# Performance work log

Hardware: AMD Instinct MI355X
Metric: run time of the kernel (lower is better)

The kernel has to match this reference:

```python
import jax, jax.numpy as jnp
import numpy as np

EMB = 1024
FF = 4 * EMB

def _ternary(w):
    # BitNet b1.58 absmean quantization; forward uses pure ternary weights
    scale = jnp.maximum(jnp.mean(jnp.abs(w)), 1e-8)
    w_t = jnp.clip(jnp.round(w / scale), -1.0, 1.0)
    # STE: forward = w_t, backward = identity w.r.t. w
    return w + jax.lax.stop_gradient(w_t - w)

def setup_inputs() -> dict:
    key = jax.random.key(0)
    kx, k1, k2, kb1, kb2 = jax.random.split(key, 5)
    x = jax.random.normal(kx, (4, 2048, EMB), dtype=jnp.float32)
    # nn.Linear default init: U(-1/sqrt(fan_in), 1/sqrt(fan_in))
    lim1 = 1.0 / np.sqrt(EMB)
    lim2 = 1.0 / np.sqrt(FF)
    W1 = jax.random.uniform(k1, (FF, EMB), jnp.float32, -lim1, lim1)
    b1 = jax.random.uniform(kb1, (FF,), jnp.float32, -lim1, lim1)
    W2 = jax.random.uniform(k2, (EMB, FF), jnp.float32, -lim2, lim2)
    b2 = jax.random.uniform(kb2, (EMB,), jnp.float32, -lim2, lim2)
    return {"x": x, "W1": W1, "b1": b1, "W2": W2, "b2": b2}

def reference(x, W1, b1, W2, b2):
    h = jnp.einsum('bsd,fd->bsf', x, _ternary(W1)) + b1  # [B,S,FF]
    h = jax.nn.gelu(h, approximate=False)  # torch nn.GELU default = exact erf
    out = jnp.einsum('bsf,df->bsd', h, _ternary(W2)) + b2  # [B,S,EMB]
    return out
```

## Files before the change

kernel.cpp:

```cpp
#include <hip/hip_runtime.h>
#include <hip/hip_bf16.h>
#include <cstdint>
#include <cstddef>

typedef __bf16 bf16x8 __attribute__((ext_vector_type(8)));
typedef float  f32x4  __attribute__((ext_vector_type(4)));

__device__ __forceinline__ unsigned short f2bf(float f) {
    __hip_bfloat16 b = __float2bfloat16(f);
    return *reinterpret_cast<unsigned short*>(&b);
}

__device__ __forceinline__ float fast_gelu(float x) {
    float x2 = x * x;
    float m  = x * __builtin_fmaf(x2, -0.10294314f, -2.30220795f);
    float e  = __builtin_amdgcn_exp2f(m);
    return x * __builtin_amdgcn_rcpf(1.0f + e);
}


__global__ void abs_sum_cvt_kernel(const float4* __restrict__ w0, const float4* __restrict__ w1,
                                   int n4w, float* __restrict__ part,
                                   const float4* __restrict__ x, ushort4* __restrict__ xb,
                                   int n4x) {
    int seg = (int)blockIdx.x >> 9;
    int b = (int)blockIdx.x & 511;
    if (seg == 2) {
        for (int i = b * blockDim.x + threadIdx.x; i < n4x; i += 512 * blockDim.x) {
            float4 v = x[i];
            ushort4 o;
            o.x = f2bf(v.x); o.y = f2bf(v.y); o.z = f2bf(v.z); o.w = f2bf(v.w);
            xb[i] = o;
        }
        return;
    }
    const float4* w = seg ? w1 : w0;
    float s = 0.0f;
    for (int i = b * blockDim.x + threadIdx.x; i < n4w; i += 512 * blockDim.x) {
        float4 v = w[i];
        s += fabsf(v.x) + fabsf(v.y) + fabsf(v.z) + fabsf(v.w);
    }
    #pragma unroll
    for (int o = 32; o > 0; o >>= 1) s += __shfl_down(s, o, 64);
    __shared__ float ps[4];
    int lane = threadIdx.x & 63, wid = threadIdx.x >> 6;
    if (lane == 0) ps[wid] = s;
    __syncthreads();
    if (threadIdx.x == 0) part[blockIdx.x] = ps[0] + ps[1] + ps[2] + ps[3];
}

__global__ void ternarize_kernel(const float4* __restrict__ w0, ushort4* __restrict__ t0,
                                 const float4* __restrict__ w1, ushort4* __restrict__ t1,
                                 int n4w, const float* __restrict__ part, float inv_n) {
    int seg = (int)blockIdx.x >> 10;
    int b = (int)blockIdx.x & 1023;

    float s = 0.0f;
    for (int j = threadIdx.x; j < 512; j += 256) s += part[seg * 512 + j];
    #pragma unroll
    for (int o = 32; o > 0; o >>= 1) s += __shfl_down(s, o, 64);
    __shared__ float ps[4];
    __shared__ float sscale;
    int lane = threadIdx.x & 63, wid = threadIdx.x >> 6;
    if (lane == 0) ps[wid] = s;
    __syncthreads();
    if (threadIdx.x == 0) {
        float tot = ps[0] + ps[1] + ps[2] + ps[3];
        sscale = fmaxf(tot * inv_n, 1e-8f);
    }
    __syncthreads();
    float inv = 1.0f / sscale;

    const float4* w = seg ? w1 : w0;
    ushort4* t = seg ? t1 : t0;
    for (int i = b * blockDim.x + threadIdx.x; i < n4w; i += 1024 * blockDim.x) {
        float4 v = w[i];
        ushort4 o;
        o.x = f2bf(fminf(fmaxf(rintf(v.x * inv), -1.0f), 1.0f));
        o.y = f2bf(fminf(fmaxf(rintf(v.y * inv), -1.0f), 1.0f));
        o.z = f2bf(fminf(fmaxf(rintf(v.z * inv), -1.0f), 1.0f));
        o.w = f2bf(fminf(fmaxf(rintf(v.w * inv), -1.0f), 1.0f));
        t[i] = o;
    }
}


#define GLL(SRC, DST) __builtin_amdgcn_global_load_lds( \
    (const __attribute__((address_space(1))) void*)(SRC), \
    (__attribute__((address_space(3))) void*)(DST), 16, 0, 0)

#define BAR() do { asm volatile("" ::: "memory"); \
    __builtin_amdgcn_sched_barrier(0); \
    __builtin_amdgcn_s_barrier(); \
    __builtin_amdgcn_sched_barrier(0); \
    asm volatile("" ::: "memory"); } while (0)

#define WAIT_LGKM() do { asm volatile("s_waitcnt lgkmcnt(0)" ::: "memory"); \
    __builtin_amdgcn_sched_barrier(0); } while (0)

#define WAIT_VM4() do { asm volatile("s_waitcnt vmcnt(4)" ::: "memory"); \
    __builtin_amdgcn_sched_barrier(0); } while (0)

#define LDA(MS, BUF) do { \
    _Pragma("unroll") \
    for (int f_ = 0; f_ < MF2; ++f_) { \
        const unsigned short* p_ = &As[(BUF)*16384 + AH*8192 + (rA0 + (MS)*(WM/2) + f_*16 + lr)*64]; \
        av[MS][f_][0] = *(const bf16x8*)(p_ + swz0); \
        av[MS][f_][1] = *(const bf16x8*)(p_ + swz1); \
    } \
} while (0)

#define LDB(NS, BUF) do { \
    _Pragma("unroll") \
    for (int g_ = 0; g_ < NF2; ++g_) { \
        const unsigned short* p_ = &Bs[(BUF)*(BN*64) + BHw*(BH*64) + (rB0 + (NS)*32 + g_*16 + lr)*64]; \
        bv[NS][g_][0] = *(const bf16x8*)(p_ + swz0); \
        bv[NS][g_][1] = *(const bf16x8*)(p_ + swz1); \
    } \
} while (0)

#define MMA(MS, NS) do { \
    __builtin_amdgcn_s_setprio(1); \
    _Pragma("unroll") \
    for (int f_ = 0; f_ < MF2; ++f_) { \
        _Pragma("unroll") \
        for (int g_ = 0; g_ < NF2; ++g_) { \
            acc[(MS)*MF2 + f_][(NS)*NF2 + g_] = __builtin_amdgcn_mfma_f32_16x16x32_bf16( \
                av[MS][f_][0], bv[NS][g_][0], acc[(MS)*MF2 + f_][(NS)*NF2 + g_], 0, 0, 0); \
            acc[(MS)*MF2 + f_][(NS)*NF2 + g_] = __builtin_amdgcn_mfma_f32_16x16x32_bf16( \
                av[MS][f_][1], bv[NS][g_][1], acc[(MS)*MF2 + f_][(NS)*NF2 + g_], 0, 0, 0); \
        } \
    } \
    __builtin_amdgcn_s_setprio(0); \
} while (0)

#define STAGE_A(BUF, H, T) do { \
    const unsigned short* s_ = pA + (size_t)((H)*128)*K + (((T) & (KT-1)) << 6); \
    GLL(s_,                 &As[(BUF)*16384 + (H)*8192 + tid*8]); \
    GLL(s_ + (size_t)64*K,  &As[(BUF)*16384 + (H)*8192 + 4096 + tid*8]); \
} while (0)

#define STAGE_B(BUF, H, T) do { \
    const unsigned short* s_ = pB + (size_t)((H)*BH)*K + (((T) & (KT-1)) << 6); \
    GLL(s_, &Bs[(BUF)*(BN*64) + (H)*(BH*64) + tid*8]); \
    if constexpr (BN == 256) { \
        GLL(s_ + (size_t)64*K, &Bs[(BUF)*(BN*64) + (H)*(BH*64) + 4096 + tid*8]); \
    } \
} while (0)

template <int EPI, int K, int N, int BN, int WM>
__global__ __launch_bounds__(512, 2)
void gemm8p_kernel(const unsigned short* __restrict__ A,
                   const unsigned short* __restrict__ B,
                   const float* __restrict__ bias,
                   void* __restrict__ C) {
    constexpr int BM = 256;
    constexpr int WN = 64;
    constexpr int WARPS_N = BN / WN;
    constexpr int MF = WM / 16;
    constexpr int NF = WN / 16;
    constexpr int MF2 = MF / 2;
    constexpr int NF2 = NF / 2;
    constexpr int BH = (BN == 256) ? 128 : 64;
    constexpr int KT = K / 64;
    constexpr int NBX = N / BN;
    static_assert((BM / WM) * WARPS_N == 8, "8 waves");
    static_assert((KT & (KT - 1)) == 0, "KT pow2");

    __shared__ __align__(16) unsigned short As[2 * 256 * 64];
    __shared__ __align__(16) unsigned short Bs[2 * BN * 64];

    const int tid  = threadIdx.x;
    const int lane = tid & 63;
    const int wid  = tid >> 6;
    const int lr = lane & 15;
    const int lq = lane >> 4;
    const int mb = wid / WARPS_N;
    const int nb = wid % WARPS_N;

    const int nwg = (int)gridDim.x;
    const int bid = (int)blockIdx.x;
    const int swz = (bid & 7) * (nwg >> 3) + (bid >> 3);
    const int bx = swz % NBX;
    const int by = swz / NBX;
    const size_t aRow0 = (size_t)by * BM;
    const size_t bRow0 = (size_t)bx * BN;

    const int sRow = tid >> 3;
    const int sChunk = ((tid & 7) ^ (sRow & 7)) << 3;
    const unsigned short* pA = A + (aRow0 + sRow) * (size_t)K + sChunk;
    const unsigned short* pB = B + (bRow0 + sRow) * (size_t)K + sChunk;

    const int swz0 = ((lq ^ (lr & 7)) << 3);
    const int swz1 = (((4 + lq) ^ (lr & 7)) << 3);
    const int AH  = (mb * WM) >> 7;
    const int rA0 = (mb * WM) & 127;
    const int BHw = (nb * WN) / BH;
    const int rB0 = (nb * WN) % BH;

    f32x4 acc[MF][NF];
    #pragma unroll
    for (int i_ = 0; i_ < MF; ++i_)
        #pragma unroll
        for (int j_ = 0; j_ < NF; ++j_)
            acc[i_][j_] = f32x4{0.f, 0.f, 0.f, 0.f};

    bf16x8 av[2][MF2][2];
    bf16x8 bv[2][NF2][2];

    STAGE_B(0, 0, 0); STAGE_B(0, 1, 0);
    STAGE_A(0, 0, 0); STAGE_A(0, 1, 0);
    STAGE_A(1, 0, 1); STAGE_A(1, 1, 1);
    WAIT_VM4();
    BAR();

    #pragma unroll 1
    for (int it = 0; it < K / 128; ++it) {
        const int tO  = 2 * it + 1;
        const int tN0 = 2 * it + 2;
        const int tN1 = 2 * it + 3;

        LDA(0, 0); LDB(0, 0);
        STAGE_B(1, 0, tO);
        BAR(); WAIT_LGKM();
        MMA(0, 0);
        BAR();

        LDA(1, 0);
        STAGE_B(1, 1, tO);
        BAR(); WAIT_LGKM();
        MMA(1, 0);
        BAR();

        LDB(1, 0);
        STAGE_A(0, 0, tN0);
        BAR(); WAIT_LGKM();
        MMA(1, 1);
        BAR();

        STAGE_A(0, 1, tN0);
        WAIT_VM4();
        BAR();
        MMA(0, 1);
        BAR();

        LDA(0, 1); LDB(0, 1);
        STAGE_B(0, 0, tN0);
        BAR(); WAIT_LGKM();
        MMA(0, 0);
        BAR();

        LDA(1, 1);
        STAGE_B(0, 1, tN0);
        BAR(); WAIT_LGKM();
        MMA(1, 0);
        BAR();

        LDB(1, 1);
        STAGE_A(1, 0, tN1);
        BAR(); WAIT_LGKM();
        MMA(1, 1);
        BAR();

        STAGE_A(1, 1, tN1);
        WAIT_VM4();
        BAR();
        MMA(0, 1);
        BAR();
    }

    #pragma unroll
    for (int mf = 0; mf < MF; ++mf) {
        #pragma unroll
        for (int nf = 0; nf < NF; ++nf) {
            const size_t col = bRow0 + (size_t)nb * WN + nf * 16 + lr;
            const float bvs = bias[col];
            #pragma unroll
            for (int r = 0; r < 4; ++r) {
                const size_t row = aRow0 + (size_t)mb * WM + mf * 16 + lq * 4 + r;
                float v = acc[mf][nf][r] + bvs;
                if constexpr (EPI == 0) {
                    ((unsigned short*)C)[row * (size_t)N + col] = f2bf(fast_gelu(v));
                } else {
                    ((float*)C)[row * (size_t)N + col] = v;
                }
            }
        }
    }
}

#undef GLL
#undef BAR
#undef WAIT_LGKM
#undef WAIT_VM4
#undef LDA
#undef LDB
#undef MMA
#undef STAGE_A
#undef STAGE_B


extern "C" void kernel_launch(void* const* d_in, const int* in_sizes, int n_in,
                              void* d_out, int out_size, void* d_ws, size_t ws_size,
                              hipStream_t stream) {
    const float* x  = (const float*)d_in[0];
    const float* W1 = (const float*)d_in[1];
    const float* b1 = (const float*)d_in[2];
    const float* W2 = (const float*)d_in[3];
    const float* b2 = (const float*)d_in[4];
    float* out = (float*)d_out;

    const int M = 8192, EMB = 1024, FF = 4096;
    const int nW = FF * EMB;

    char* ws = (char*)d_ws;
    float* part = (float*)ws;
    unsigned short* W1t = (unsigned short*)(ws + 16384);
    unsigned short* W2t = W1t + (size_t)nW;
    unsigned short* xb  = W2t + (size_t)nW;
    unsigned short* h   = xb  + (size_t)M * EMB;

    abs_sum_cvt_kernel<<<1536, 256, 0, stream>>>((const float4*)W1, (const float4*)W2,
                                                 nW / 4, part,
                                                 (const float4*)x, (ushort4*)xb,
                                                 (M * EMB) / 4);
    ternarize_kernel<<<2048, 256, 0, stream>>>((const float4*)W1, (ushort4*)W1t,
                                               (const float4*)W2, (ushort4*)W2t,
                                               nW / 4, part, 1.0f / nW);

    gemm8p_kernel<0, 1024, 4096, 256, 128><<<dim3(512), dim3(512), 0, stream>>>(xb, W1t, b1, h);
    gemm8p_kernel<1, 4096, 1024, 128, 64><<<dim3(256), dim3(512), 0, stream>>>(h, W2t, b2, out);
}
```

Baseline: 268.6 us.

## Prefetch LDS fragments one MMA phase ahead with partial waitcnt pipelining

Restructures the 8-phase GEMM main loop so each phase issues the LDS reads for the next MMA sub-tile while the current one computes, and replaces full lgkmcnt(0) waits with partial counts. The first fragment load is hoisted before the loop, and the MMA quadrant order is rearranged (a snake order that reuses already-loaded fragments). vmcnt waits are redistributed per phase depending on the B staging width. This targets exposed LDS latency between MMA blocks, at the cost of fragile hand-counted wait values and higher register pressure from extra live fragments.

New measurement: 282.3 us. +5.1%, slower.

```diff
diff --git a/kernel.cpp b/kernel.cpp
--- a/kernel.cpp
+++ b/kernel.cpp
@@ -95,11 +95,15 @@
     __builtin_amdgcn_sched_barrier(0); \
     asm volatile("" ::: "memory"); } while (0)
 
-#define WAIT_LGKM() do { asm volatile("s_waitcnt lgkmcnt(0)" ::: "memory"); \
+#define WLG_N(NN) do { asm volatile("s_waitcnt lgkmcnt(" #NN ")" ::: "memory"); \
     __builtin_amdgcn_sched_barrier(0); } while (0)
-
-#define WAIT_VM4() do { asm volatile("s_waitcnt vmcnt(4)" ::: "memory"); \
+#define WVM_N(NN) do { asm volatile("s_waitcnt vmcnt(" #NN ")" ::: "memory"); \
     __builtin_amdgcn_sched_barrier(0); } while (0)
+
+#define WLG_A() do { if constexpr (MF2 == 4) WLG_N(8); else WLG_N(4); } while (0)
+#define WLG_B() WLG_N(4)
+#define WVM_B1()   do { if constexpr (SBL == 2) WVM_N(6); else WVM_N(5); } while (0)
+#define WVM_HALF() do { if constexpr (SBL == 2) WVM_N(2); else WVM_N(1); } while (0)
 
 #define LDA(MS, BUF) do { \
     _Pragma("unroll") \
@@ -162,6 +166,7 @@
     constexpr int MF2 = MF / 2;
     constexpr int NF2 = NF / 2;
     constexpr int BH = (BN == 256) ? 128 : 64;
+    constexpr int SBL = (BN == 256) ? 2 : 1;
     constexpr int KT = K / 64;
     constexpr int NBX = N / BN;
     static_assert((BM / WM) * WARPS_N == 8, "8 waves");
@@ -211,61 +216,54 @@
     STAGE_B(0, 0, 0); STAGE_B(0, 1, 0);
     STAGE_A(0, 0, 0); STAGE_A(0, 1, 0);
     STAGE_A(1, 0, 1); STAGE_A(1, 1, 1);
-    WAIT_VM4();
+    WVM_N(4);
     BAR();
+    LDA(0, 0); LDB(0, 0);
 
     #pragma unroll 1
     for (int it = 0; it < K / 128; ++it) {
-        const int tO  = 2 * it + 1;
-        const int tN0 = 2 * it + 2;
-        const int tN1 = 2 * it + 3;
-
-        LDA(0, 0); LDB(0, 0);
-        STAGE_B(1, 0, tO);
-        BAR(); WAIT_LGKM();
+        const int t1 = 2 * it + 1;
+        const int t2 = 2 * it + 2;
+        const int t3 = 2 * it + 3;
+
+        LDA(1, 0); STAGE_B(1, 0, t1);
+        BAR(); WLG_A();
         MMA(0, 0);
-        BAR();
-
-        LDA(1, 0);
-        STAGE_B(1, 1, tO);
-        BAR(); WAIT_LGKM();
+        WVM_B1(); BAR();
+
+        LDB(1, 0); STAGE_B(1, 1, t1);
+        BAR(); WLG_B();
         MMA(1, 0);
-        BAR();
-
-        LDB(1, 0);
-        STAGE_A(0, 0, tN0);
-        BAR(); WAIT_LGKM();
+        WVM_HALF(); BAR();
+
+        LDB(0, 1); STAGE_A(0, 0, t2);
+        BAR(); WLG_B();
         MMA(1, 1);
         BAR();
 
-        STAGE_A(0, 1, tN0);
-        WAIT_VM4();
-        BAR();
+        LDA(1, 1); STAGE_A(0, 1, t2);
+        BAR(); WLG_A();
         MMA(0, 1);
         BAR();
 
-        LDA(0, 1); LDB(0, 1);
-        STAGE_B(0, 0, tN0);
-        BAR(); WAIT_LGKM();
+        LDA(0, 1); STAGE_B(0, 0, t2);
+        BAR(); WLG_A();
+        MMA(1, 0);
+        WVM_B1(); BAR();
+
+        LDB(1, 1); STAGE_B(0, 1, t2);
+        BAR(); WLG_B();
         MMA(0, 0);
+        WVM_HALF(); BAR();
+
+        LDB(0, 0); STAGE_A(1, 0, t3);
+        BAR(); WLG_B();
+        MMA(0, 1);
         BAR();
 
-        LDA(1, 1);
-        STAGE_B(0, 1, tN0);
-        BAR(); WAIT_LGKM();
-        MMA(1, 0);
-        BAR();
-
-        LDB(1, 1);
-        STAGE_A(1, 0, tN1);
-        BAR(); WAIT_LGKM();
+        LDA(0, 0); STAGE_A(1, 1, t3);
+        BAR(); WLG_A();
         MMA(1, 1);
-        BAR();
-
-        STAGE_A(1, 1, tN1);
-        WAIT_VM4();
-        BAR();
-        MMA(0, 1);
         BAR();
     }
 
@@ -291,8 +289,12 @@
 
 #undef GLL
 #undef BAR
-#undef WAIT_LGKM
-#undef WAIT_VM4
+#undef WLG_N
+#undef WVM_N
+#undef WLG_A
+#undef WLG_B
+#undef WVM_B1
+#undef WVM_HALF
 #undef LDA
 #undef LDB
 #undef MMA
```

## Prefetch B tiles a full step earlier and move vmcnt wait after MMA

Applied to the files above, without the earlier changes.

Restructures the software pipeline so the B operand halves are staged earlier, issued alongside the A stages for the following tile rather than just before use. The vmcnt wait moves to after the last MMA of each half-iteration, with counts adjusted by the B tile width, and a final full drain is added before the epilogue. The intent is to hide more global-to-LDS latency behind MFMA work. The cost is more outstanding loads, and any mistake in buffer reuse or wait counts would cause data races.

Result: faster. 258.0 us (-4.0%).

```diff
diff --git a/kernel.cpp b/kernel.cpp
--- a/kernel.cpp
+++ b/kernel.cpp
@@ -95,11 +95,11 @@
     __builtin_amdgcn_sched_barrier(0); \
     asm volatile("" ::: "memory"); } while (0)
 
-#define WAIT_LGKM() do { asm volatile("s_waitcnt lgkmcnt(0)" ::: "memory"); \
+#define WLG0() do { asm volatile("s_waitcnt lgkmcnt(0)" ::: "memory"); \
     __builtin_amdgcn_sched_barrier(0); } while (0)
-
-#define WAIT_VM4() do { asm volatile("s_waitcnt vmcnt(4)" ::: "memory"); \
+#define WVM_N(NN) do { asm volatile("s_waitcnt vmcnt(" #NN ")" ::: "memory"); \
     __builtin_amdgcn_sched_barrier(0); } while (0)
+#define WVM_TILE() do { if constexpr (SBL == 2) WVM_N(6); else WVM_N(5); } while (0)
 
 #define LDA(MS, BUF) do { \
     _Pragma("unroll") \
@@ -140,7 +140,7 @@
     GLL(s_ + (size_t)64*K,  &As[(BUF)*16384 + (H)*8192 + 4096 + tid*8]); \
 } while (0)
 
-#define STAGE_B(BUF, H, T) do { \
+#define STAGE_BH(BUF, H, T) do { \
     const unsigned short* s_ = pB + (size_t)((H)*BH)*K + (((T) & (KT-1)) << 6); \
     GLL(s_, &Bs[(BUF)*(BN*64) + (H)*(BH*64) + tid*8]); \
     if constexpr (BN == 256) { \
@@ -162,6 +162,7 @@
     constexpr int MF2 = MF / 2;
     constexpr int NF2 = NF / 2;
     constexpr int BH = (BN == 256) ? 128 : 64;
+    constexpr int SBL = (BN == 256) ? 2 : 1;
     constexpr int KT = K / 64;
     constexpr int NBX = N / BN;
     static_assert((BM / WM) * WARPS_N == 8, "8 waves");
@@ -208,66 +209,65 @@
     bf16x8 av[2][MF2][2];
     bf16x8 bv[2][NF2][2];
 
-    STAGE_B(0, 0, 0); STAGE_B(0, 1, 0);
-    STAGE_A(0, 0, 0); STAGE_A(0, 1, 0);
-    STAGE_A(1, 0, 1); STAGE_A(1, 1, 1);
-    WAIT_VM4();
+    STAGE_A(0, 0, 0); STAGE_A(0, 1, 0); STAGE_BH(0, 0, 0); STAGE_BH(0, 1, 0);
+    STAGE_A(1, 0, 1); STAGE_A(1, 1, 1); STAGE_BH(1, 0, 1);
+    WVM_TILE();
     BAR();
 
     #pragma unroll 1
     for (int it = 0; it < K / 128; ++it) {
-        const int tO  = 2 * it + 1;
-        const int tN0 = 2 * it + 2;
-        const int tN1 = 2 * it + 3;
+        const int t1 = 2 * it + 1;
+        const int t2 = 2 * it + 2;
+        const int t3 = 2 * it + 3;
 
         LDA(0, 0); LDB(0, 0);
-        STAGE_B(1, 0, tO);
-        BAR(); WAIT_LGKM();
+        STAGE_BH(1, 1, t1);
+        BAR(); WLG0();
         MMA(0, 0);
         BAR();
 
         LDA(1, 0);
-        STAGE_B(1, 1, tO);
-        BAR(); WAIT_LGKM();
+        BAR(); WLG0();
         MMA(1, 0);
         BAR();
 
         LDB(1, 0);
-        STAGE_A(0, 0, tN0);
-        BAR(); WAIT_LGKM();
+        STAGE_A(0, 0, t2);
+        BAR(); WLG0();
         MMA(1, 1);
         BAR();
 
-        STAGE_A(0, 1, tN0);
-        WAIT_VM4();
+        STAGE_A(0, 1, t2); STAGE_BH(0, 0, t2);
         BAR();
         MMA(0, 1);
+        WVM_TILE();
         BAR();
 
         LDA(0, 1); LDB(0, 1);
-        STAGE_B(0, 0, tN0);
-        BAR(); WAIT_LGKM();
+        STAGE_BH(0, 1, t2);
+        BAR(); WLG0();
         MMA(0, 0);
         BAR();
 
         LDA(1, 1);
-        STAGE_B(0, 1, tN0);
-        BAR(); WAIT_LGKM();
+        BAR(); WLG0();
         MMA(1, 0);
         BAR();
 
         LDB(1, 1);
-        STAGE_A(1, 0, tN1);
-        BAR(); WAIT_LGKM();
+        STAGE_A(1, 0, t3);
+        BAR(); WLG0();
         MMA(1, 1);
         BAR();
 
-        STAGE_A(1, 1, tN1);
-        WAIT_VM4();
+        STAGE_A(1, 1, t3); STAGE_BH(1, 0, t3);
         BAR();
         MMA(0, 1);
-        BAR();
-    }
+        WVM_TILE();
+        BAR();
+    }
+
+    WVM_N(0);
 
     #pragma unroll
     for (int mf = 0; mf < MF; ++mf) {
@@ -291,13 +291,14 @@
 
 #undef GLL
 #undef BAR
-#undef WAIT_LGKM
-#undef WAIT_VM4
+#undef WLG0
+#undef WVM_N
+#undef WVM_TILE
 #undef LDA
 #undef LDB
 #undef MMA
 #undef STAGE_A
-#undef STAGE_B
+#undef STAGE_BH
 
 
 extern "C" void kernel_launch(void* const* d_in, const int* in_sizes, int n_in,
```
